# Kernel tuning notes

Hardware: AMD Instinct MI355X
Metric: run time of the kernel (lower is better)

Reference implementation:

```python
import jax, jax.numpy as jnp
import numpy as np

B, T, E = 8, 2048, 512   # batch, tokens, embedding_dim
K, C = 8192, 8           # num_embeddings, codebook_dim
LN_EPS = 1e-5


def _layer_norm(x, g, b):
    mu = jnp.mean(x, axis=-1, keepdims=True)
    var = jnp.var(x, axis=-1, keepdims=True)
    return (x - mu) * jax.lax.rsqrt(var + LN_EPS) * g + b


def setup_inputs() -> dict:
    key = jax.random.key(0)
    ks = jax.random.split(key, 8)
    s_e = 1.0 / np.sqrt(E)
    s_c = 1.0 / np.sqrt(C)
    return {
        "features": jax.random.normal(ks[0], (B, T, E), dtype=jnp.float32),
        # project_in: Linear(E,E) -> ReLU -> Linear(E,C)
        "W1_in": jax.random.uniform(ks[1], (E, E), jnp.float32, -s_e, s_e),
        "b1_in": jnp.zeros((E,), jnp.float32),
        "W2_in": jax.random.uniform(ks[2], (E, C), jnp.float32, -s_e, s_e),
        "b2_in": jnp.zeros((C,), jnp.float32),
        "ln_in_g": jnp.ones((C,), jnp.float32),
        "ln_in_b": jnp.zeros((C,), jnp.float32),
        # codebook
        "emb": jax.random.normal(ks[3], (K, C), dtype=jnp.float32),
        # project_out: Linear(C,E) -> ReLU -> Linear(E,E)
        "W1_out": jax.random.uniform(ks[4], (C, E), jnp.float32, -s_c, s_c),
        "b1_out": jnp.zeros((E,), jnp.float32),
        "W2_out": jax.random.uniform(ks[5], (E, E), jnp.float32, -s_e, s_e),
        "b2_out": jnp.zeros((E,), jnp.float32),
        "ln_out_g": jnp.ones((E,), jnp.float32),
        "ln_out_b": jnp.zeros((E,), jnp.float32),
    }


def reference(features, W1_in, b1_in, W2_in, b2_in, ln_in_g, ln_in_b, emb,
              W1_out, b1_out, W2_out, b2_out, ln_out_g, ln_out_b):
    # project_in + norm_in
    h = jax.nn.relu(jnp.einsum('bte,ef->btf', features, W1_in) + b1_in)
    z = jnp.einsum('bte,ec->btc', h, W2_in) + b2_in          # (B,T,C)
    z = _layer_norm(z, ln_in_g, ln_in_b)
    zf = z.reshape(-1, C)                                     # (N,C)
    d = (jnp.sum(zf * zf, axis=1, keepdims=True)
         - 2.0 * zf @ emb.T
         + jnp.sum(emb * emb, axis=1)[None, :])               # (N,K)
    idx = jnp.argmin(d, axis=1)                               # (N,)
    encodings = jax.nn.one_hot(idx, K, dtype=zf.dtype)        # (N,K)
    quantized = emb[idx]                                      # gather == one_hot @ emb
    # project_out + norm_out
    q = jax.nn.relu(quantized @ W1_out + b1_out)
    q = q @ W2_out + b2_out
    q = _layer_norm(q, ln_out_g, ln_out_b)
    q = q.reshape(B, T, E)
    return q, idx[:, None], encodings
```

## Files before the change

kernel.cpp:

```cpp
#include <hip/hip_runtime.h>
#include <cstdint>
#include <cstddef>

#define N_TOK 16384
#define E_DIM 512
#define C_DIM 8
#define K_CODES 8192
#define LN_EPS 1e-5f

typedef __attribute__((ext_vector_type(8))) short short8;
typedef __attribute__((ext_vector_type(4))) float f32x4;

__device__ __forceinline__ unsigned short bf16_rn(float x) {
  unsigned u = __float_as_uint(x);
  unsigned r = u + 0x7FFFu + ((u >> 16) & 1u);
  return (unsigned short)(r >> 16);
}
__device__ __forceinline__ float bf16_f(unsigned short h) {
  return __uint_as_float(((unsigned)h) << 16);
}

__device__ __forceinline__ void gload16(const void* g, void* l) {
  __builtin_amdgcn_global_load_lds(
      (const __attribute__((address_space(1))) void*)g,
      (__attribute__((address_space(3))) void*)l, 16, 0, 0);
}

__device__ __forceinline__ void pack_a_body(const float* __restrict__ A,
    unsigned short* __restrict__ hi, unsigned short* __restrict__ lo, int t) {
  int l = t & 63;
  int kt = (t >> 6) & 15;
  int mf = t >> 10;
  const float* src = A + (size_t)(mf * 16 + (l & 15)) * 512 + kt * 32 + (l >> 4) * 8;
  float4 x0 = *(const float4*)src;
  float4 x1 = *(const float4*)(src + 4);
  float xs[8] = {x0.x, x0.y, x0.z, x0.w, x1.x, x1.y, x1.z, x1.w};
  unsigned hw[4], lw[4];
#pragma unroll
  for (int p = 0; p < 4; ++p) {
    float a = xs[2 * p], b = xs[2 * p + 1];
    unsigned short ha = bf16_rn(a), hb = bf16_rn(b);
    unsigned short la = bf16_rn(a - bf16_f(ha)), lb = bf16_rn(b - bf16_f(hb));
    hw[p] = (unsigned)ha | ((unsigned)hb << 16);
    lw[p] = (unsigned)la | ((unsigned)lb << 16);
  }
  uint4 hv; hv.x = hw[0]; hv.y = hw[1]; hv.z = hw[2]; hv.w = hw[3];
  uint4 lv; lv.x = lw[0]; lv.y = lw[1]; lv.z = lw[2]; lv.w = lw[3];
  ((uint4*)hi)[t] = hv;
  ((uint4*)lo)[t] = lv;
}

__device__ __forceinline__ void pack_b_body(const float* __restrict__ B,
    unsigned short* __restrict__ hi, unsigned short* __restrict__ lo, int t) {
  int l = t & 63;
  int kt = (t >> 6) & 15;
  int nf = t >> 10;
  int col = nf * 16 + (l & 15);
  int krow = kt * 32 + (l >> 4) * 8;
  unsigned hw[4], lw[4];
#pragma unroll
  for (int p = 0; p < 4; ++p) {
    float a = B[(size_t)(krow + 2 * p) * 512 + col];
    float b = B[(size_t)(krow + 2 * p + 1) * 512 + col];
    unsigned short ha = bf16_rn(a), hb = bf16_rn(b);
    unsigned short la = bf16_rn(a - bf16_f(ha)), lb = bf16_rn(b - bf16_f(hb));
    hw[p] = (unsigned)ha | ((unsigned)hb << 16);
    lw[p] = (unsigned)la | ((unsigned)lb << 16);
  }
  uint4 hv; hv.x = hw[0]; hv.y = hw[1]; hv.z = hw[2]; hv.w = hw[3];
  uint4 lv; lv.x = lw[0]; lv.y = lw[1]; lv.z = lw[2]; lv.w = lw[3];
  ((uint4*)hi)[t] = hv;
  ((uint4*)lo)[t] = lv;
}

__global__ __launch_bounds__(256) void prep(const float* __restrict__ features,
    const float* __restrict__ W1_in, const float* __restrict__ W2_out,
    const float* __restrict__ emb,
    const float* __restrict__ W1_out, const float* __restrict__ b1_out,
    unsigned short* __restrict__ A1h, unsigned short* __restrict__ A1l,
    unsigned short* __restrict__ B1h, unsigned short* __restrict__ B1l,
    unsigned short* __restrict__ B2h, unsigned short* __restrict__ B2l,
    unsigned short* __restrict__ A2h, unsigned short* __restrict__ A2l,
    float* __restrict__ ne) {
  int bid = blockIdx.x;
  int tid = threadIdx.x;
  if (bid < 4096) {
    pack_a_body(features, A1h, A1l, bid * 256 + tid);
  } else if (bid < 4224) {
    pack_b_body(W1_in, B1h, B1l, (bid - 4096) * 256 + tid);
  } else if (bid < 4352) {
    pack_b_body(W2_out, B2h, B2l, (bid - 4224) * 256 + tid);
  } else if (bid < 4384) {
    int k = (bid - 4352) * 256 + tid;
    const float* e = emb + (size_t)k * C_DIM;
    float s = 0.f;
#pragma unroll
    for (int c = 0; c < C_DIM; ++c) s = fmaf(e[c], e[c], s);
    ne[k] = s;
  } else {
    int mf = bid - 4384;
    int l = tid & 63;
    int kt4 = tid >> 6;
    int k0 = mf * 16 + (l & 15);
    float ev[C_DIM];
#pragma unroll
    for (int c = 0; c < C_DIM; ++c) ev[c] = emb[(size_t)k0 * C_DIM + c];
#pragma unroll
    for (int it = 0; it < 4; ++it) {
      int kt = it * 4 + kt4;
      int e0 = kt * 32 + (l >> 4) * 8;
      float o[8];
      float4 bv0 = *(const float4*)(b1_out + e0);
      float4 bv1 = *(const float4*)(b1_out + e0 + 4);
      o[0] = bv0.x; o[1] = bv0.y; o[2] = bv0.z; o[3] = bv0.w;
      o[4] = bv1.x; o[5] = bv1.y; o[6] = bv1.z; o[7] = bv1.w;
#pragma unroll
      for (int c = 0; c < C_DIM; ++c) {
        float4 w0 = *(const float4*)(W1_out + (size_t)c * E_DIM + e0);
        float4 w1 = *(const float4*)(W1_out + (size_t)c * E_DIM + e0 + 4);
        o[0] = fmaf(ev[c], w0.x, o[0]); o[1] = fmaf(ev[c], w0.y, o[1]);
        o[2] = fmaf(ev[c], w0.z, o[2]); o[3] = fmaf(ev[c], w0.w, o[3]);
        o[4] = fmaf(ev[c], w1.x, o[4]); o[5] = fmaf(ev[c], w1.y, o[5]);
        o[6] = fmaf(ev[c], w1.z, o[6]); o[7] = fmaf(ev[c], w1.w, o[7]);
      }
      unsigned hw[4], lw[4];
#pragma unroll
      for (int p = 0; p < 4; ++p) {
        float a = fmaxf(o[2 * p], 0.f), b = fmaxf(o[2 * p + 1], 0.f);
        unsigned short ha = bf16_rn(a), hb = bf16_rn(b);
        unsigned short la = bf16_rn(a - bf16_f(ha)), lb = bf16_rn(b - bf16_f(hb));
        hw[p] = (unsigned)ha | ((unsigned)hb << 16);
        lw[p] = (unsigned)la | ((unsigned)lb << 16);
      }
      size_t t = ((size_t)mf * 16 + kt) * 64 + l;
      uint4 hv; hv.x = hw[0]; hv.y = hw[1]; hv.z = hw[2]; hv.w = hw[3];
      uint4 lv; lv.x = lw[0]; lv.y = lw[1]; lv.z = lw[2]; lv.w = lw[3];
      ((uint4*)A2h)[t] = hv;
      ((uint4*)A2l)[t] = lv;
    }
  }
}

template<bool RELU>
__global__ __launch_bounds__(256) void gemm_mfma(const unsigned short* __restrict__ Ah,
    const unsigned short* __restrict__ Al, const unsigned short* __restrict__ Bh,
    const unsigned short* __restrict__ Bl, const float* __restrict__ bias,
    float* __restrict__ C) {
  __shared__ char smem[65536];
  const int tid = threadIdx.x;
  const int l = tid & 63;
  const int w = tid >> 6;
  const int wm = w >> 1, wn = w & 1;
  const int mblk = blockIdx.y, nblk = blockIdx.x;

  const char* gAh = (const char*)Ah + (((size_t)(mblk * 8 + 2 * w) * 16) * 64 + l) * 16;
  const char* gAl = (const char*)Al + (((size_t)(mblk * 8 + 2 * w) * 16) * 64 + l) * 16;
  const char* gBh = (const char*)Bh + (((size_t)(nblk * 8 + 2 * w) * 16) * 64 + l) * 16;
  const char* gBl = (const char*)Bl + (((size_t)(nblk * 8 + 2 * w) * 16) * 64 + l) * 16;

  f32x4 acc[4][4];
#pragma unroll
  for (int i = 0; i < 4; ++i)
#pragma unroll
    for (int j = 0; j < 4; ++j) acc[i][j] = (f32x4){0.f, 0.f, 0.f, 0.f};

  auto stage = [&](int buf, int kt) {
    char* base = smem + buf * 32768;
    const size_t ko = (size_t)kt * 1024;
    char* dA0 = base + (2 * w) * 1024;
    char* dA1 = base + 8192 + (2 * w) * 1024;
    char* dB0 = base + 16384 + (2 * w) * 1024;
    char* dB1 = base + 24576 + (2 * w) * 1024;
    gload16(gAh + ko,         dA0);
    gload16(gAh + ko + 16384, dA0 + 1024);
    gload16(gAl + ko,         dA1);
    gload16(gAl + ko + 16384, dA1 + 1024);
    gload16(gBh + ko,         dB0);
    gload16(gBh + ko + 16384, dB0 + 1024);
    gload16(gBl + ko,         dB1);
    gload16(gBl + ko + 16384, dB1 + 1024);
  };

  auto compute = [&](int buf) {
    const char* base = smem + buf * 32768;
    const short8* sAh = (const short8*)(base);
    const short8* sAl = (const short8*)(base + 8192);
    const short8* sBh = (const short8*)(base + 16384);
    const short8* sBl = (const short8*)(base + 24576);
    short8 a_h[4], a_l[4], b_h[4], b_l[4];
#pragma unroll
    for (int i = 0; i < 4; ++i) {
      a_h[i] = sAh[(wm * 4 + i) * 64 + l];
      a_l[i] = sAl[(wm * 4 + i) * 64 + l];
    }
#pragma unroll
    for (int j = 0; j < 4; ++j) {
      b_h[j] = sBh[(wn * 4 + j) * 64 + l];
      b_l[j] = sBl[(wn * 4 + j) * 64 + l];
    }
#pragma unroll
    for (int i = 0; i < 4; ++i)
#pragma unroll
      for (int j = 0; j < 4; ++j)
        acc[i][j] = __builtin_amdgcn_mfma_f32_16x16x32_bf16(a_h[i], b_h[j], acc[i][j], 0, 0, 0);
#pragma unroll
    for (int i = 0; i < 4; ++i)
#pragma unroll
      for (int j = 0; j < 4; ++j)
        acc[i][j] = __builtin_amdgcn_mfma_f32_16x16x32_bf16(a_h[i], b_l[j], acc[i][j], 0, 0, 0);
#pragma unroll
    for (int i = 0; i < 4; ++i)
#pragma unroll
      for (int j = 0; j < 4; ++j)
        acc[i][j] = __builtin_amdgcn_mfma_f32_16x16x32_bf16(a_l[i], b_h[j], acc[i][j], 0, 0, 0);
  };

  stage(0, 0);
  __syncthreads();
  int cur = 0;
#pragma unroll 1
  for (int kt = 1; kt < 16; ++kt) {
    stage(cur ^ 1, kt);
    compute(cur);
    __syncthreads();
    cur ^= 1;
  }
  compute(cur);

  const int colb = nblk * 128 + wn * 64 + (l & 15);
  const int rowb = mblk * 128 + wm * 64 + ((l >> 4) << 2);
#pragma unroll
  for (int j = 0; j < 4; ++j) {
    float bv = bias[colb + j * 16];
#pragma unroll
    for (int i = 0; i < 4; ++i) {
#pragma unroll
      for (int r = 0; r < 4; ++r) {
        float v = acc[i][j][r] + bv;
        if (RELU) v = fmaxf(v, 0.f);
        C[(size_t)(rowb + i * 16 + r) * 512 + colb + j * 16] = v;
      }
    }
  }
}

__global__ __launch_bounds__(256) void zln_kernel(const float* __restrict__ h,
    const float* __restrict__ W2, const float* __restrict__ b2,
    const float* __restrict__ g, const float* __restrict__ b,
    float* __restrict__ z) {
  int token = blockIdx.x * 4 + (threadIdx.x >> 6);
  int lane = threadIdx.x & 63;
  const float* hr = h + (size_t)token * E_DIM;
  float acc[C_DIM];
#pragma unroll
  for (int c = 0; c < C_DIM; ++c) acc[c] = 0.f;
  for (int e = lane; e < E_DIM; e += 64) {
    float hv = hr[e];
    const float* w = W2 + e * C_DIM;
#pragma unroll
    for (int c = 0; c < C_DIM; ++c) acc[c] = fmaf(hv, w[c], acc[c]);
  }
#pragma unroll
  for (int c = 0; c < C_DIM; ++c) {
#pragma unroll
    for (int off = 32; off > 0; off >>= 1) acc[c] += __shfl_down(acc[c], off);
  }
  if (lane == 0) {
    float v[C_DIM]; float mu = 0.f;
#pragma unroll
    for (int c = 0; c < C_DIM; ++c) { v[c] = acc[c] + b2[c]; mu += v[c]; }
    mu *= 0.125f;
    float var = 0.f;
#pragma unroll
    for (int c = 0; c < C_DIM; ++c) { float d = v[c] - mu; var += d * d; }
    var *= 0.125f;
    float inv = 1.0f / sqrtf(var + LN_EPS);
#pragma unroll
    for (int c = 0; c < C_DIM; ++c)
      z[(size_t)token * C_DIM + c] = ((v[c] - mu) * inv) * g[c] + b[c];
  }
}

__global__ __launch_bounds__(256) void vq_partial(const float* __restrict__ z,
    const float* __restrict__ emb, const float* __restrict__ ne,
    float* __restrict__ pbest, int* __restrict__ pidx, float4* __restrict__ zb) {
  int chunk = blockIdx.x & 7;
  int token = (blockIdx.x >> 3) * 256 + threadIdx.x;
  float zv[C_DIM];
#pragma unroll
  for (int c = 0; c < C_DIM; ++c) zv[c] = z[(size_t)token * C_DIM + c];
  float s = 0.f;
#pragma unroll
  for (int c = 0; c < C_DIM; ++c) s = fmaf(zv[c], zv[c], s);
  float best = 3.402823466e38f; int bi = 0;
  int j0 = chunk * 1024;
  const size_t zbase = (size_t)blockIdx.x * 65536 + threadIdx.x;
  float4 z4 = {0.f, 0.f, 0.f, 0.f};
#pragma unroll 1
  for (int jo = 0; jo < 64; ++jo) {
    if (zb) {
#pragma unroll
      for (int su = 0; su < 4; ++su)
        zb[zbase + (size_t)(jo * 4 + su) * 256] = z4;
    }
#pragma unroll
    for (int ji = 0; ji < 16; ++ji) {
      int j = j0 + jo * 16 + ji;
      const float* e = emb + (size_t)j * C_DIM;
      float p = 0.f;
#pragma unroll
      for (int c = 0; c < C_DIM; ++c) p = fmaf(zv[c], e[c], p);
      float d = fmaf(-2.f, p, s) + ne[j];
      if (d < best) { best = d; bi = j; }
    }
  }
  pbest[chunk * N_TOK + token] = best;
  pidx[chunk * N_TOK + token] = bi;
}

__global__ __launch_bounds__(128) void gather_ln(const float* __restrict__ oc,
    const float* __restrict__ pbest, const int* __restrict__ pidx,
    const float* __restrict__ gw, const float* __restrict__ bw,
    float* __restrict__ q, float* __restrict__ idxf, float* __restrict__ enc_plant) {
  int n = blockIdx.x;
  int tid = threadIdx.x;
  float best = pbest[n]; int k = pidx[n];
#pragma unroll
  for (int c = 1; c < 8; ++c) {
    float bb = pbest[c * N_TOK + n]; int i2 = pidx[c * N_TOK + n];
    if (bb < best) { best = bb; k = i2; }
  }
  const float* r = oc + (size_t)k * E_DIM;
  float4 v = ((const float4*)r)[tid];
  __shared__ float red[4];
  int lane = tid & 63, wid = tid >> 6;
  float sum = v.x + v.y + v.z + v.w;
#pragma unroll
  for (int off = 32; off > 0; off >>= 1) sum += __shfl_xor(sum, off);
  if (lane == 0) red[wid] = sum;
  __syncthreads();
  float mu = (red[0] + red[1]) * (1.0f / 512.0f);
  float4 d;
  d.x = v.x - mu; d.y = v.y - mu; d.z = v.z - mu; d.w = v.w - mu;
  float sq = d.x * d.x + d.y * d.y + d.z * d.z + d.w * d.w;
#pragma unroll
  for (int off = 32; off > 0; off >>= 1) sq += __shfl_xor(sq, off);
  if (lane == 0) red[2 + wid] = sq;
  __syncthreads();
  float var = (red[2] + red[3]) * (1.0f / 512.0f);
  float inv = 1.0f / sqrtf(var + LN_EPS);
  float4 gg = ((const float4*)gw)[tid];
  float4 bb = ((const float4*)bw)[tid];
  float4 o;
  o.x = d.x * inv * gg.x + bb.x;
  o.y = d.y * inv * gg.y + bb.y;
  o.z = d.z * inv * gg.z + bb.z;
  o.w = d.w * inv * gg.w + bb.w;
  ((float4*)(q + (size_t)n * E_DIM))[tid] = o;
  if (tid == 0) {
    idxf[n] = (float)k;
    if (enc_plant) enc_plant[(size_t)n * K_CODES + k] = 1.0f;
  }
}

__global__ __launch_bounds__(256) void zero_scatter(const float* __restrict__ idxf,
    float* __restrict__ enc) {
  int n = blockIdx.x;
  int tid = threadIdx.x;
  int k = (int)idxf[n];
  float* row = enc + (size_t)n * K_CODES;
  float4 zv = {0.f, 0.f, 0.f, 0.f};
#pragma unroll
  for (int u = 0; u < 8; ++u)
    ((float4*)row)[u * 256 + tid] = zv;
  if (((k >> 2) & 255) == tid) row[k] = 1.0f;
}

extern "C" void kernel_launch(void* const* d_in, const int* in_sizes, int n_in,
                              void* d_out, int out_size, void* d_ws, size_t ws_size,
                              hipStream_t stream) {
  const float* features = (const float*)d_in[0];
  const float* W1_in  = (const float*)d_in[1];
  const float* b1_in  = (const float*)d_in[2];
  const float* W2_in  = (const float*)d_in[3];
  const float* b2_in  = (const float*)d_in[4];
  const float* ln_in_g = (const float*)d_in[5];
  const float* ln_in_b = (const float*)d_in[6];
  const float* emb    = (const float*)d_in[7];
  const float* W1_out = (const float*)d_in[8];
  const float* b1_out = (const float*)d_in[9];
  const float* W2_out = (const float*)d_in[10];
  const float* b2_out = (const float*)d_in[11];
  const float* ln_out_g = (const float*)d_in[12];
  const float* ln_out_b = (const float*)d_in[13];

  float* q    = (float*)d_out;
  float* idxf = q + (size_t)N_TOK * E_DIM;
  float* enc  = idxf + N_TOK;

  const size_t WS_NEED = 26091520ULL * 4ULL;
  const bool use_ws = (d_ws != nullptr) && (ws_size >= WS_NEED);

  float *h, *g, *z, *ne, *pbest; int* pidx;
  unsigned short *A1h, *A1l, *A2h, *A2l, *B1h, *B1l, *B2h, *B2l;
  if (use_ws) {
    float* ws = (float*)d_ws;
    h     = ws;
    g     = ws + 8388608;
    z     = ws + 12582912;
    ne    = ws + 12713984;
    pbest = ws + 12722176;
    pidx  = (int*)(ws + 12853248);
    A1h = (unsigned short*)(ws + 12984320);
    A1l = (unsigned short*)(ws + 17178624);
    A2h = (unsigned short*)(ws + 21372928);
    A2l = (unsigned short*)(ws + 23470080);
    B1h = (unsigned short*)(ws + 25567232);
    B1l = (unsigned short*)(ws + 25698304);
    B2h = (unsigned short*)(ws + 25829376);
    B2l = (unsigned short*)(ws + 25960448);
  } else {
    h     = enc;
    g     = enc + 12582912;
    z     = enc + 16777216;
    ne    = enc + 16908288;
    pbest = enc + 16916480;
    pidx  = (int*)(enc + 17063936);
    A1h = (unsigned short*)(enc + 17195008);
    A1l = (unsigned short*)(enc + 21389312);
    A2h = (unsigned short*)(enc + 25583616);
    A2l = (unsigned short*)(enc + 27680768);
    B1h = (unsigned short*)(enc + 29777920);
    B1l = (unsigned short*)(enc + 29908992);
    B2h = (unsigned short*)(enc + 30040064);
    B2l = (unsigned short*)(enc + 30171136);
  }

  float4* zbv   = use_ws ? (float4*)enc : nullptr;
  float*  plant = use_ws ? enc : nullptr;

  prep<<<4896, 256, 0, stream>>>(features, W1_in, W2_out, emb, W1_out, b1_out,
                                 A1h, A1l, B1h, B1l, B2h, B2l, A2h, A2l, ne);

  dim3 g1(4, N_TOK / 128);
  gemm_mfma<true><<<g1, 256, 0, stream>>>(A1h, A1l, B1h, B1l, b1_in, h);

  zln_kernel<<<N_TOK / 4, 256, 0, stream>>>(h, W2_in, b2_in, ln_in_g, ln_in_b, z);

  vq_partial<<<(N_TOK / 256) * 8, 256, 0, stream>>>(z, emb, ne, pbest, pidx, zbv);

  dim3 g2(4, K_CODES / 128);
  gemm_mfma<false><<<g2, 256, 0, stream>>>(A2h, A2l, B2h, B2l, b2_out, g);

  gather_ln<<<N_TOK, 128, 0, stream>>>(g, pbest, pidx, ln_out_g, ln_out_b,
                                       q, idxf, plant);

  if (!use_ws) {
    zero_scatter<<<N_TOK, 256, 0, stream>>>(idxf, enc);
  }
}
```

Baseline: 831.4 us.

## Use 512-thread GEMM blocks, drop fused encoding zeroing from VQ search

The split-bf16 MFMA GEMM moves from 4 to 8 waves per block. Each wave now stages one 1KB slice per operand and computes a 4x2 tile instead of 4x4, which is meant to add latency hiding and lower register pressure. The one-hot zero-fill that was interleaved into the VQ argmin loop, and the plant write in gather_ln, are removed. A separate zero_scatter kernel now always writes the full encodings matrix, which likely costs an extra full pass over the 512MB output in exchange for a simpler pipeline.

```diff
diff --git a/kernel.cpp b/kernel.cpp
--- a/kernel.cpp
+++ b/kernel.cpp
@@ -142,7 +142,7 @@
 }
 
 template<bool RELU>
-__global__ __launch_bounds__(256) void gemm_mfma(const unsigned short* __restrict__ Ah,
+__global__ __launch_bounds__(512, 4) void gemm_mfma(const unsigned short* __restrict__ Ah,
     const unsigned short* __restrict__ Al, const unsigned short* __restrict__ Bh,
     const unsigned short* __restrict__ Bl, const float* __restrict__ bias,
     float* __restrict__ C) {
@@ -150,35 +150,28 @@
   const int tid = threadIdx.x;
   const int l = tid & 63;
   const int w = tid >> 6;
-  const int wm = w >> 1, wn = w & 1;
+  const int wm = w >> 2;
+  const int wn = w & 3;
   const int mblk = blockIdx.y, nblk = blockIdx.x;
 
-  const char* gAh = (const char*)Ah + (((size_t)(mblk * 8 + 2 * w) * 16) * 64 + l) * 16;
-  const char* gAl = (const char*)Al + (((size_t)(mblk * 8 + 2 * w) * 16) * 64 + l) * 16;
-  const char* gBh = (const char*)Bh + (((size_t)(nblk * 8 + 2 * w) * 16) * 64 + l) * 16;
-  const char* gBl = (const char*)Bl + (((size_t)(nblk * 8 + 2 * w) * 16) * 64 + l) * 16;
-
-  f32x4 acc[4][4];
+  const char* gAh = (const char*)Ah + (((size_t)(mblk * 8 + w) * 16) * 64 + l) * 16;
+  const char* gAl = (const char*)Al + (((size_t)(mblk * 8 + w) * 16) * 64 + l) * 16;
+  const char* gBh = (const char*)Bh + (((size_t)(nblk * 8 + w) * 16) * 64 + l) * 16;
+  const char* gBl = (const char*)Bl + (((size_t)(nblk * 8 + w) * 16) * 64 + l) * 16;
+
+  f32x4 acc[4][2];
 #pragma unroll
   for (int i = 0; i < 4; ++i)
 #pragma unroll
-    for (int j = 0; j < 4; ++j) acc[i][j] = (f32x4){0.f, 0.f, 0.f, 0.f};
+    for (int j = 0; j < 2; ++j) acc[i][j] = (f32x4){0.f, 0.f, 0.f, 0.f};
 
   auto stage = [&](int buf, int kt) {
     char* base = smem + buf * 32768;
     const size_t ko = (size_t)kt * 1024;
-    char* dA0 = base + (2 * w) * 1024;
-    char* dA1 = base + 8192 + (2 * w) * 1024;
-    char* dB0 = base + 16384 + (2 * w) * 1024;
-    char* dB1 = base + 24576 + (2 * w) * 1024;
-    gload16(gAh + ko,         dA0);
-    gload16(gAh + ko + 16384, dA0 + 1024);
-    gload16(gAl + ko,         dA1);
-    gload16(gAl + ko + 16384, dA1 + 1024);
-    gload16(gBh + ko,         dB0);
-    gload16(gBh + ko + 16384, dB0 + 1024);
-    gload16(gBl + ko,         dB1);
-    gload16(gBl + ko + 16384, dB1 + 1024);
+    gload16(gAh + ko, base + w * 1024);
+    gload16(gAl + ko, base + 8192 + w * 1024);
+    gload16(gBh + ko, base + 16384 + w * 1024);
+    gload16(gBl + ko, base + 24576 + w * 1024);
   };
 
   auto compute = [&](int buf) {
@@ -187,31 +180,31 @@
     const short8* sAl = (const short8*)(base + 8192);
     const short8* sBh = (const short8*)(base + 16384);
     const short8* sBl = (const short8*)(base + 24576);
-    short8 a_h[4], a_l[4], b_h[4], b_l[4];
+    short8 a_h[4], a_l[4], b_h[2], b_l[2];
 #pragma unroll
     for (int i = 0; i < 4; ++i) {
       a_h[i] = sAh[(wm * 4 + i) * 64 + l];
       a_l[i] = sAl[(wm * 4 + i) * 64 + l];
     }
 #pragma unroll
-    for (int j = 0; j < 4; ++j) {
-      b_h[j] = sBh[(wn * 4 + j) * 64 + l];
-      b_l[j] = sBl[(wn * 4 + j) * 64 + l];
+    for (int j = 0; j < 2; ++j) {
+      b_h[j] = sBh[(wn * 2 + j) * 64 + l];
+      b_l[j] = sBl[(wn * 2 + j) * 64 + l];
     }
 #pragma unroll
     for (int i = 0; i < 4; ++i)
 #pragma unroll
-      for (int j = 0; j < 4; ++j)
+      for (int j = 0; j < 2; ++j)
         acc[i][j] = __builtin_amdgcn_mfma_f32_16x16x32_bf16(a_h[i], b_h[j], acc[i][j], 0, 0, 0);
 #pragma unroll
     for (int i = 0; i < 4; ++i)
 #pragma unroll
-      for (int j = 0; j < 4; ++j)
+      for (int j = 0; j < 2; ++j)
         acc[i][j] = __builtin_amdgcn_mfma_f32_16x16x32_bf16(a_h[i], b_l[j], acc[i][j], 0, 0, 0);
 #pragma unroll
     for (int i = 0; i < 4; ++i)
 #pragma unroll
-      for (int j = 0; j < 4; ++j)
+      for (int j = 0; j < 2; ++j)
         acc[i][j] = __builtin_amdgcn_mfma_f32_16x16x32_bf16(a_l[i], b_h[j], acc[i][j], 0, 0, 0);
   };
 
@@ -227,10 +220,10 @@
   }
   compute(cur);
 
-  const int colb = nblk * 128 + wn * 64 + (l & 15);
+  const int colb = nblk * 128 + wn * 32 + (l & 15);
   const int rowb = mblk * 128 + wm * 64 + ((l >> 4) << 2);
 #pragma unroll
-  for (int j = 0; j < 4; ++j) {
+  for (int j = 0; j < 2; ++j) {
     float bv = bias[colb + j * 16];
 #pragma unroll
     for (int i = 0; i < 4; ++i) {
@@ -283,7 +276,7 @@
 
 __global__ __launch_bounds__(256) void vq_partial(const float* __restrict__ z,
     const float* __restrict__ emb, const float* __restrict__ ne,
-    float* __restrict__ pbest, int* __restrict__ pidx, float4* __restrict__ zb) {
+    float* __restrict__ pbest, int* __restrict__ pidx) {
   int chunk = blockIdx.x & 7;
   int token = (blockIdx.x >> 3) * 256 + threadIdx.x;
   float zv[C_DIM];
@@ -294,25 +287,13 @@
   for (int c = 0; c < C_DIM; ++c) s = fmaf(zv[c], zv[c], s);
   float best = 3.402823466e38f; int bi = 0;
   int j0 = chunk * 1024;
-  const size_t zbase = (size_t)blockIdx.x * 65536 + threadIdx.x;
-  float4 z4 = {0.f, 0.f, 0.f, 0.f};
-#pragma unroll 1
-  for (int jo = 0; jo < 64; ++jo) {
-    if (zb) {
-#pragma unroll
-      for (int su = 0; su < 4; ++su)
-        zb[zbase + (size_t)(jo * 4 + su) * 256] = z4;
-    }
-#pragma unroll
-    for (int ji = 0; ji < 16; ++ji) {
-      int j = j0 + jo * 16 + ji;
-      const float* e = emb + (size_t)j * C_DIM;
-      float p = 0.f;
-#pragma unroll
-      for (int c = 0; c < C_DIM; ++c) p = fmaf(zv[c], e[c], p);
-      float d = fmaf(-2.f, p, s) + ne[j];
-      if (d < best) { best = d; bi = j; }
-    }
+  for (int j = j0; j < j0 + 1024; ++j) {
+    const float* e = emb + (size_t)j * C_DIM;
+    float p = 0.f;
+#pragma unroll
+    for (int c = 0; c < C_DIM; ++c) p = fmaf(zv[c], e[c], p);
+    float d = fmaf(-2.f, p, s) + ne[j];
+    if (d < best) { best = d; bi = j; }
   }
   pbest[chunk * N_TOK + token] = best;
   pidx[chunk * N_TOK + token] = bi;
@@ -321,7 +302,7 @@
 __global__ __launch_bounds__(128) void gather_ln(const float* __restrict__ oc,
     const float* __restrict__ pbest, const int* __restrict__ pidx,
     const float* __restrict__ gw, const float* __restrict__ bw,
-    float* __restrict__ q, float* __restrict__ idxf, float* __restrict__ enc_plant) {
+    float* __restrict__ q, float* __restrict__ idxf) {
   int n = blockIdx.x;
   int tid = threadIdx.x;
   float best = pbest[n]; int k = pidx[n];
@@ -357,10 +338,7 @@
   o.z = d.z * inv * gg.z + bb.z;
   o.w = d.w * inv * gg.w + bb.w;
   ((float4*)(q + (size_t)n * E_DIM))[tid] = o;
-  if (tid == 0) {
-    idxf[n] = (float)k;
-    if (enc_plant) enc_plant[(size_t)n * K_CODES + k] = 1.0f;
-  }
+  if (tid == 0) idxf[n] = (float)k;
 }
 
 __global__ __launch_bounds__(256) void zero_scatter(const float* __restrict__ idxf,
@@ -436,26 +414,20 @@
     B2l = (unsigned short*)(enc + 30171136);
   }
 
-  float4* zbv   = use_ws ? (float4*)enc : nullptr;
-  float*  plant = use_ws ? enc : nullptr;
-
   prep<<<4896, 256, 0, stream>>>(features, W1_in, W2_out, emb, W1_out, b1_out,
                                  A1h, A1l, B1h, B1l, B2h, B2l, A2h, A2l, ne);
 
   dim3 g1(4, N_TOK / 128);
-  gemm_mfma<true><<<g1, 256, 0, stream>>>(A1h, A1l, B1h, B1l, b1_in, h);
+  gemm_mfma<true><<<g1, 512, 0, stream>>>(A1h, A1l, B1h, B1l, b1_in, h);
 
   zln_kernel<<<N_TOK / 4, 256, 0, stream>>>(h, W2_in, b2_in, ln_in_g, ln_in_b, z);
 
-  vq_partial<<<(N_TOK / 256) * 8, 256, 0, stream>>>(z, emb, ne, pbest, pidx, zbv);
+  vq_partial<<<(N_TOK / 256) * 8, 256, 0, stream>>>(z, emb, ne, pbest, pidx);
 
   dim3 g2(4, K_CODES / 128);
-  gemm_mfma<false><<<g2, 256, 0, stream>>>(A2h, A2l, B2h, B2l, b2_out, g);
-
-  gather_ln<<<N_TOK, 128, 0, stream>>>(g, pbest, pidx, ln_out_g, ln_out_b,
-                                       q, idxf, plant);
-
-  if (!use_ws) {
-    zero_scatter<<<N_TOK, 256, 0, stream>>>(idxf, enc);
-  }
-}
+  gemm_mfma<false><<<g2, 512, 0, stream>>>(A2h, A2l, B2h, B2l, b2_out, g);
+
+  gather_ln<<<N_TOK, 128, 0, stream>>>(g, pbest, pidx, ln_out_g, ln_out_b, q, idxf);
+
+  zero_scatter<<<N_TOK, 256, 0, stream>>>(idxf, enc);
+}
```

Measured after the change: 786.3 us. -5.4%, faster.
